# Kernel optimization log

Hardware: AMD Instinct MI355X
Metric: run time of the kernel (lower is better)

Reference implementation:

```python
import jax, jax.numpy as jnp
import numpy as np

EXPR_MASK_RATIO = 0.4
POS_MASK_RATIO = 0.33
MIN_VISIBLE_GENES = 10


def setup_inputs() -> dict:
    key = jax.random.key(0)
    k1, k2 = jax.random.split(key)
    expression = jax.random.normal(k1, (16, 1024, 2000), dtype=jnp.float32)
    position = jax.random.normal(k2, (16, 1024, 3), dtype=jnp.float32)
    return {"expression": expression, "position": position}


def _expression_mask(expression, key):
    # strategy == 'random': rand matrix, kthvalue threshold, mask = rand >= threshold
    B, N, G = expression.shape
    num_masked = max(1, int(G * EXPR_MASK_RATIO))
    num_masked = min(num_masked, G - MIN_VISIBLE_GENES)
    rand = jax.random.uniform(key, (B, N, G), dtype=jnp.float32)
    # torch.kthvalue(rand, G - num_masked): (G - num_masked)-th smallest value,
    # i.e. index G - num_masked - 1 of the ascending sort (keepdim=True).
    kth = jnp.sort(rand, axis=-1)[..., G - num_masked - 1 : G - num_masked]  # (B,N,1)
    return rand >= kth  # bool (B,N,G); includes the threshold element, as in torch code


def _position_mask(position, key):
    # Vectorized form of the per-(b,n) loop:
    #   r < ratio*0.3      -> mask 2 of 3 dims (randperm(3)[:2] == complement of one uniform dim)
    #   ratio*0.3 <= r < ratio -> mask 1 uniform dim
    B, N, _ = position.shape
    kr, k1, k2 = jax.random.split(key, 3)
    r = jax.random.uniform(kr, (B, N), dtype=jnp.float32)
    two = r < POS_MASK_RATIO * 0.3
    one = (r < POS_MASK_RATIO) & (~two)
    dim1 = jax.random.randint(k1, (B, N), 0, 3)  # dim masked in the 1-dim branch
    excl = jax.random.randint(k2, (B, N), 0, 3)  # dim kept in the 2-dim branch
    eye = jnp.eye(3, dtype=bool)
    m1 = eye[dim1]        # (B,N,3) one-hot
    m2 = ~eye[excl]       # (B,N,3) two hot
    false3 = jnp.zeros((B, N, 3), dtype=bool)
    return jnp.where(two[..., None], m2, jnp.where(one[..., None], m1, false3))


def reference(expression, position):
    key = jax.random.key(42)
    ke, kp = jax.random.split(key)
    expr_mask = _expression_mask(expression, ke)   # (B,N,G) bool
    pos_mask = _position_mask(position, kp)        # (B,N,3) bool
    return expr_mask, pos_mask
```

## Files before the change

### kernel.cpp

```cpp
#include <hip/hip_runtime.h>
#include <stdint.h>

#define TF_ROUND(x0, x1, r)                    \
  {                                            \
    x0 += x1;                                  \
    x1 = (x1 << (r)) | (x1 >> (32 - (r)));     \
    x1 ^= x0;                                  \
  }

__host__ __device__ inline void threefry2x32(uint32_t k0, uint32_t k1,
                                             uint32_t x0, uint32_t x1,
                                             uint32_t& o0, uint32_t& o1) {
  const uint32_t ks2 = k0 ^ k1 ^ 0x1BD11BDAu;
  x0 += k0; x1 += k1;
  TF_ROUND(x0, x1, 13) TF_ROUND(x0, x1, 15) TF_ROUND(x0, x1, 26) TF_ROUND(x0, x1, 6)
  x0 += k1; x1 += ks2 + 1u;
  TF_ROUND(x0, x1, 17) TF_ROUND(x0, x1, 29) TF_ROUND(x0, x1, 16) TF_ROUND(x0, x1, 24)
  x0 += ks2; x1 += k0 + 2u;
  TF_ROUND(x0, x1, 13) TF_ROUND(x0, x1, 15) TF_ROUND(x0, x1, 26) TF_ROUND(x0, x1, 6)
  x0 += k0; x1 += k1 + 3u;
  TF_ROUND(x0, x1, 17) TF_ROUND(x0, x1, 29) TF_ROUND(x0, x1, 16) TF_ROUND(x0, x1, 24)
  x0 += k1; x1 += ks2 + 4u;
  TF_ROUND(x0, x1, 13) TF_ROUND(x0, x1, 15) TF_ROUND(x0, x1, 26) TF_ROUND(x0, x1, 6)
  x0 += ks2; x1 += k0 + 5u;
  o0 = x0; o1 = x1;
}

__device__ inline uint32_t random_bits32(uint32_t k0, uint32_t k1, uint32_t i) {
  uint32_t y0, y1;
  threefry2x32(k0, k1, 0u, i, y0, y1);
  return y0 ^ y1;
}

constexpr int B = 16;
constexpr int N = 1024;
constexpr int G = 2000;
constexpr int NUM_ROWS = B * N;
constexpr int RANK = G - 800 - 1;
constexpr long long EXPR_ELEMS = (long long)NUM_ROWS * G;
constexpr int PER_THREAD = 8;
constexpr int ACTIVE_T = G / PER_THREAD;

__global__ __launch_bounds__(256) void expr_mask_kernel(int32_t* __restrict__ out,
                                                        uint32_t ke0,
                                                        uint32_t ke1) {
  __shared__ uint32_t hist[256];
  __shared__ uint32_t scan[256];
  __shared__ uint32_t cand[256];
  __shared__ uint32_t s_cnt;
  __shared__ uint32_t s_bucket;
  __shared__ uint32_t s_kk;
  __shared__ uint32_t s_thr;

  const int t = threadIdx.x;
  const uint32_t rowstart = (uint32_t)blockIdx.x * (uint32_t)G;
  const uint32_t base = rowstart + (uint32_t)t * (uint32_t)PER_THREAD;
  const bool active = (t < ACTIVE_T);

  hist[t] = 0u;
  if (t == 0) s_cnt = 0u;
  __syncthreads();

  uint32_t m[PER_THREAD];
  if (active) {
#pragma unroll
    for (int j = 0; j < PER_THREAD; ++j) {
      uint32_t bits = random_bits32(ke0, ke1, base + (uint32_t)j);
      m[j] = bits >> 9;
      atomicAdd(&hist[m[j] >> 15], 1u);
    }
  }
  __syncthreads();

  uint32_t v = hist[t];
  scan[t] = v;
  __syncthreads();
  for (int off = 1; off < 256; off <<= 1) {
    uint32_t add = (t >= off) ? scan[t - off] : 0u;
    __syncthreads();
    scan[t] += add;
    __syncthreads();
  }
  uint32_t incl = scan[t];
  uint32_t excl = incl - v;
  if (excl <= (uint32_t)RANK && (uint32_t)RANK < incl) {
    s_bucket = (uint32_t)t;
    s_kk = (uint32_t)RANK - excl;
  }
  __syncthreads();

  const uint32_t bucket = s_bucket;
  if (active) {
#pragma unroll
    for (int j = 0; j < PER_THREAD; ++j) {
      if ((m[j] >> 15) == bucket) {
        uint32_t p = atomicAdd(&s_cnt, 1u);
        if (p < 256u) cand[p] = m[j];
      }
    }
  }
  __syncthreads();

  const uint32_t c = (s_cnt < 256u) ? s_cnt : 256u;
  const uint32_t kk = s_kk;
  if ((uint32_t)t < c) {
    uint32_t mv = cand[t];
    uint32_t r = 0;
    for (uint32_t j = 0; j < c; ++j) {
      uint32_t mj = cand[j];
      r += (mj < mv) || (mj == mv && j < (uint32_t)t);
    }
    if (r == kk) s_thr = mv;
  }
  __syncthreads();

  const uint32_t thr = s_thr;
  if (active) {
    int4 a, b;
    a.x = (m[0] >= thr) ? 1 : 0;
    a.y = (m[1] >= thr) ? 1 : 0;
    a.z = (m[2] >= thr) ? 1 : 0;
    a.w = (m[3] >= thr) ? 1 : 0;
    b.x = (m[4] >= thr) ? 1 : 0;
    b.y = (m[5] >= thr) ? 1 : 0;
    b.z = (m[6] >= thr) ? 1 : 0;
    b.w = (m[7] >= thr) ? 1 : 0;
    int4* p = (int4*)(out + base);
    p[0] = a;
    p[1] = b;
  }
}

__global__ __launch_bounds__(256) void pos_mask_kernel(
    int32_t* __restrict__ out,
    uint32_t kr0, uint32_t kr1,
    uint32_t ah0, uint32_t ah1, uint32_t al0, uint32_t al1,
    uint32_t bh0, uint32_t bh1, uint32_t bl0, uint32_t bl1) {
  const int i = blockIdx.x * 256 + threadIdx.x;
  if (i >= NUM_ROWS) return;

  uint32_t rb = random_bits32(kr0, kr1, (uint32_t)i);
  union { uint32_t u; float f; } cvt;
  cvt.u = (rb >> 9) | 0x3F800000u;
  float r = cvt.f - 1.0f;

  const float THR2 = (float)(0.33 * 0.3);
  const float THR1 = (float)0.33;
  bool two = r < THR2;
  bool one = (r < THR1) && !two;

  uint32_t ah = random_bits32(ah0, ah1, (uint32_t)i);
  uint32_t al = random_bits32(al0, al1, (uint32_t)i);
  int dim1 = (int)(((ah % 3u) + (al % 3u)) % 3u);

  uint32_t bh = random_bits32(bh0, bh1, (uint32_t)i);
  uint32_t bl = random_bits32(bl0, bl1, (uint32_t)i);
  int excl = (int)(((bh % 3u) + (bl % 3u)) % 3u);

  int o[3];
#pragma unroll
  for (int d = 0; d < 3; ++d) {
    bool mval = two ? (d != excl) : (one ? (d == dim1) : false);
    o[d] = mval ? 1 : 0;
  }
  long long obase = (long long)i * 3;
  out[obase + 0] = o[0];
  out[obase + 1] = o[1];
  out[obase + 2] = o[2];
}

extern "C" void kernel_launch(void* const* d_in, const int* in_sizes, int n_in,
                              void* d_out, int out_size, void* d_ws, size_t ws_size,
                              hipStream_t stream) {
  (void)d_in; (void)in_sizes; (void)n_in; (void)d_ws; (void)ws_size; (void)out_size;

  uint32_t ke0, ke1, kp0, kp1;
  threefry2x32(0u, 42u, 0u, 0u, ke0, ke1);
  threefry2x32(0u, 42u, 0u, 1u, kp0, kp1);
  uint32_t kr0, kr1, ka0, ka1, kb0, kb1;
  threefry2x32(kp0, kp1, 0u, 0u, kr0, kr1);
  threefry2x32(kp0, kp1, 0u, 1u, ka0, ka1);
  threefry2x32(kp0, kp1, 0u, 2u, kb0, kb1);
  uint32_t ah0, ah1, al0, al1, bh0, bh1, bl0, bl1;
  threefry2x32(ka0, ka1, 0u, 0u, ah0, ah1);
  threefry2x32(ka0, ka1, 0u, 1u, al0, al1);
  threefry2x32(kb0, kb1, 0u, 0u, bh0, bh1);
  threefry2x32(kb0, kb1, 0u, 1u, bl0, bl1);

  int32_t* out_expr = (int32_t*)d_out;
  int32_t* out_pos = out_expr + EXPR_ELEMS;

  expr_mask_kernel<<<NUM_ROWS, 256, 0, stream>>>(out_expr, ke0, ke1);
  pos_mask_kernel<<<(NUM_ROWS + 255) / 256, 256, 0, stream>>>(
      out_pos, kr0, kr1, ah0, ah1, al0, al1, bh0, bh1, bl0, bl1);
}
```

Measured before the change: 246.0 us.

## Fuse position mask into expression kernel, use wave-shuffle scan and nontemporal stores

Merges the position-mask kernel into the expression-mask kernel. Idle threads (250-254) compute the per-row position random bits and thread 255 writes the three position flags, which removes a separate launch. The 8-step shared-memory Hillis-Steele scan with its many barriers is replaced by a single-wavefront shuffle scan over 4 histogram bins per lane. Output stores become nontemporal to avoid cache pollution. Extra branch logic in the idle lanes adds a little work per block but should overlap with the main threefry computation.

Measured after the change: 242.4 us. Within noise of the previous version (-1.5%).

```diff
diff --git a/kernel.cpp b/kernel.cpp
--- a/kernel.cpp
+++ b/kernel.cpp
@@ -36,25 +36,30 @@
 constexpr int N = 1024;
 constexpr int G = 2000;
 constexpr int NUM_ROWS = B * N;
-constexpr int RANK = G - 800 - 1;
+constexpr uint32_t RANK = (uint32_t)(G - 800 - 1);
 constexpr long long EXPR_ELEMS = (long long)NUM_ROWS * G;
 constexpr int PER_THREAD = 8;
 constexpr int ACTIVE_T = G / PER_THREAD;
 
-__global__ __launch_bounds__(256) void expr_mask_kernel(int32_t* __restrict__ out,
-                                                        uint32_t ke0,
-                                                        uint32_t ke1) {
-  __shared__ uint32_t hist[256];
-  __shared__ uint32_t scan[256];
+typedef int v4i __attribute__((ext_vector_type(4)));
+
+__global__ __launch_bounds__(256) void fused_mask_kernel(
+    int32_t* __restrict__ out_expr, int32_t* __restrict__ out_pos,
+    uint32_t ke0, uint32_t ke1,
+    uint32_t kr0, uint32_t kr1,
+    uint32_t ah0, uint32_t ah1, uint32_t al0, uint32_t al1,
+    uint32_t bh0, uint32_t bh1, uint32_t bl0, uint32_t bl1) {
+  __shared__ alignas(16) uint32_t hist[256];
   __shared__ uint32_t cand[256];
+  __shared__ uint32_t s_posbits[5];
   __shared__ uint32_t s_cnt;
   __shared__ uint32_t s_bucket;
   __shared__ uint32_t s_kk;
   __shared__ uint32_t s_thr;
 
   const int t = threadIdx.x;
-  const uint32_t rowstart = (uint32_t)blockIdx.x * (uint32_t)G;
-  const uint32_t base = rowstart + (uint32_t)t * (uint32_t)PER_THREAD;
+  const uint32_t row = blockIdx.x;
+  const uint32_t base = row * (uint32_t)G + (uint32_t)t * (uint32_t)PER_THREAD;
   const bool active = (t < ACTIVE_T);
 
   hist[t] = 0u;
@@ -69,23 +74,53 @@
       m[j] = bits >> 9;
       atomicAdd(&hist[m[j] >> 15], 1u);
     }
+  } else if (t < 255) {
+    uint32_t pk0, pk1;
+    switch (t) {
+      case 250: pk0 = kr0; pk1 = kr1; break;
+      case 251: pk0 = ah0; pk1 = ah1; break;
+      case 252: pk0 = al0; pk1 = al1; break;
+      case 253: pk0 = bh0; pk1 = bh1; break;
+      default:  pk0 = bl0; pk1 = bl1; break;
+    }
+    s_posbits[t - 250] = random_bits32(pk0, pk1, row);
   }
   __syncthreads();
 
-  uint32_t v = hist[t];
-  scan[t] = v;
-  __syncthreads();
-  for (int off = 1; off < 256; off <<= 1) {
-    uint32_t add = (t >= off) ? scan[t - off] : 0u;
-    __syncthreads();
-    scan[t] += add;
-    __syncthreads();
-  }
-  uint32_t incl = scan[t];
-  uint32_t excl = incl - v;
-  if (excl <= (uint32_t)RANK && (uint32_t)RANK < incl) {
-    s_bucket = (uint32_t)t;
-    s_kk = (uint32_t)RANK - excl;
+  if (t < 64) {
+    uint4 h = reinterpret_cast<const uint4*>(hist)[t];
+    uint32_t tot = h.x + h.y + h.z + h.w;
+    uint32_t x = tot;
+#pragma unroll
+    for (int d = 1; d < 64; d <<= 1) {
+      uint32_t o = __shfl_up(x, d, 64);
+      if (t >= d) x += o;
+    }
+    uint32_t e0 = x - tot;
+    uint32_t e1 = e0 + h.x;
+    uint32_t e2 = e1 + h.y;
+    uint32_t e3 = e2 + h.z;
+    if (e0 <= RANK && RANK < e1) { s_bucket = 4u * t + 0u; s_kk = RANK - e0; }
+    if (e1 <= RANK && RANK < e2) { s_bucket = 4u * t + 1u; s_kk = RANK - e1; }
+    if (e2 <= RANK && RANK < e3) { s_bucket = 4u * t + 2u; s_kk = RANK - e2; }
+    if (e3 <= RANK && RANK < e3 + h.w) { s_bucket = 4u * t + 3u; s_kk = RANK - e3; }
+  } else if (t == 255) {
+    uint32_t rb = s_posbits[0];
+    union { uint32_t u; float f; } cvt;
+    cvt.u = (rb >> 9) | 0x3F800000u;
+    float r = cvt.f - 1.0f;
+    const float THR2 = (float)(0.33 * 0.3);
+    const float THR1 = (float)0.33;
+    bool two = r < THR2;
+    bool one = (r < THR1) && !two;
+    int dim1 = (int)(((s_posbits[1] % 3u) + (s_posbits[2] % 3u)) % 3u);
+    int excl = (int)(((s_posbits[3] % 3u) + (s_posbits[4] % 3u)) % 3u);
+    uint32_t obase = row * 3u;
+#pragma unroll
+    for (int d = 0; d < 3; ++d) {
+      bool mval = two ? (d != excl) : (one ? (d == dim1) : false);
+      out_pos[obase + (uint32_t)d] = mval ? 1 : 0;
+    }
   }
   __syncthreads();
 
@@ -116,7 +151,7 @@
 
   const uint32_t thr = s_thr;
   if (active) {
-    int4 a, b;
+    v4i a, b;
     a.x = (m[0] >= thr) ? 1 : 0;
     a.y = (m[1] >= thr) ? 1 : 0;
     a.z = (m[2] >= thr) ? 1 : 0;
@@ -125,48 +160,10 @@
     b.y = (m[5] >= thr) ? 1 : 0;
     b.z = (m[6] >= thr) ? 1 : 0;
     b.w = (m[7] >= thr) ? 1 : 0;
-    int4* p = (int4*)(out + base);
-    p[0] = a;
-    p[1] = b;
+    v4i* p = (v4i*)(out_expr + base);
+    __builtin_nontemporal_store(a, p);
+    __builtin_nontemporal_store(b, p + 1);
   }
-}
-
-__global__ __launch_bounds__(256) void pos_mask_kernel(
-    int32_t* __restrict__ out,
-    uint32_t kr0, uint32_t kr1,
-    uint32_t ah0, uint32_t ah1, uint32_t al0, uint32_t al1,
-    uint32_t bh0, uint32_t bh1, uint32_t bl0, uint32_t bl1) {
-  const int i = blockIdx.x * 256 + threadIdx.x;
-  if (i >= NUM_ROWS) return;
-
-  uint32_t rb = random_bits32(kr0, kr1, (uint32_t)i);
-  union { uint32_t u; float f; } cvt;
-  cvt.u = (rb >> 9) | 0x3F800000u;
-  float r = cvt.f - 1.0f;
-
-  const float THR2 = (float)(0.33 * 0.3);
-  const float THR1 = (float)0.33;
-  bool two = r < THR2;
-  bool one = (r < THR1) && !two;
-
-  uint32_t ah = random_bits32(ah0, ah1, (uint32_t)i);
-  uint32_t al = random_bits32(al0, al1, (uint32_t)i);
-  int dim1 = (int)(((ah % 3u) + (al % 3u)) % 3u);
-
-  uint32_t bh = random_bits32(bh0, bh1, (uint32_t)i);
-  uint32_t bl = random_bits32(bl0, bl1, (uint32_t)i);
-  int excl = (int)(((bh % 3u) + (bl % 3u)) % 3u);
-
-  int o[3];
-#pragma unroll
-  for (int d = 0; d < 3; ++d) {
-    bool mval = two ? (d != excl) : (one ? (d == dim1) : false);
-    o[d] = mval ? 1 : 0;
-  }
-  long long obase = (long long)i * 3;
-  out[obase + 0] = o[0];
-  out[obase + 1] = o[1];
-  out[obase + 2] = o[2];
 }
 
 extern "C" void kernel_launch(void* const* d_in, const int* in_sizes, int n_in,
@@ -190,7 +187,7 @@
   int32_t* out_expr = (int32_t*)d_out;
   int32_t* out_pos = out_expr + EXPR_ELEMS;
 
-  expr_mask_kernel<<<NUM_ROWS, 256, 0, stream>>>(out_expr, ke0, ke1);
-  pos_mask_kernel<<<(NUM_ROWS + 255) / 256, 256, 0, stream>>>(
-      out_pos, kr0, kr1, ah0, ah1, al0, al1, bh0, bh1, bl0, bl1);
+  fused_mask_kernel<<<NUM_ROWS, 256, 0, stream>>>(
+      out_expr, out_pos, ke0, ke1, kr0, kr1,
+      ah0, ah1, al0, al1, bh0, bh1, bl0, bl1);
 }
```
